# Optimization experiments

Measured on AMD Instinct MI355X. Metric: run time of the kernel, lower is better.

The kernel has to match this reference:

```python
import jax, jax.numpy as jnp
import numpy as np

B, D = 4096, 1024
NA, NNEG = 2048, 4094
L2_WEIGHT = 0.005


def setup_inputs() -> dict:
    key = jax.random.key(0)
    k1, k2, k3, k4 = jax.random.split(key, 4)
    batch = jax.random.normal(k1, (B, D), dtype=jnp.float32)
    anchors = jax.random.randint(k2, (NA,), 0, B)
    positives = jax.random.randint(k3, (NA,), 0, B)
    negatives = jax.random.randint(k4, (NA, NNEG), 0, B)
    return {"batch": batch, "anchors": anchors, "positives": positives, "negatives": negatives}


def reference(batch, anchors, positives, negatives):
    # a . (n - p) = a.n - a.p  -> one GEMM against the whole batch, then gathers.
    a_embs = batch[anchors]                       # [Na, D]
    scores = a_embs @ batch.T                     # [Na, B]
    pos = jnp.take_along_axis(scores, positives[:, None], axis=1)   # [Na, 1]
    neg = jnp.take_along_axis(scores, negatives, axis=1)            # [Na, Nneg]
    inner = neg - pos                             # [Na, Nneg]
    npair = jnp.mean(jnp.log(jnp.sum(jnp.exp(inner), axis=1) + 1.0))
    # per-anchor l2 term: l2_weight * mean(||batch||) added len(anchors) times / len(anchors)
    l2 = L2_WEIGHT * jnp.mean(jnp.linalg.norm(batch, axis=1))
    return npair + l2
```

## Files before the change

### kernel.cpp

```cpp
#include <hip/hip_runtime.h>
#include <hip/hip_bf16.h>
#include <math.h>

constexpr int kB    = 4096;
constexpr int kD    = 1024;
constexpr int kNA   = 2048;
constexpr int kNNEG = 4094;
constexpr float kL2W = 0.005f;


typedef __attribute__((ext_vector_type(8))) short short8;
typedef __attribute__((ext_vector_type(4))) float f32x4;

__device__ inline void async_load16(const void* g, void* l) {
    __builtin_amdgcn_global_load_lds(
        (const __attribute__((address_space(1))) unsigned*)g,
        (__attribute__((address_space(3))) unsigned*)l, 16, 0, 0);
}
__device__ inline float bf16_to_f(unsigned short u) {
    union { unsigned int i; float f; } c; c.i = ((unsigned int)u) << 16; return c.f;
}

__global__ __launch_bounds__(256) void conv_norms_kernel(
    const float* __restrict__ batch,
    unsigned short* __restrict__ bf,
    float* __restrict__ norms)
{
    const int row = blockIdx.x, t = threadIdx.x;
    const float4 v = ((const float4*)(batch + (size_t)row * kD))[t];
    ushort4 o;
    __hip_bfloat16 h0 = __float2bfloat16(v.x); o.x = *(unsigned short*)&h0;
    __hip_bfloat16 h1 = __float2bfloat16(v.y); o.y = *(unsigned short*)&h1;
    __hip_bfloat16 h2 = __float2bfloat16(v.z); o.z = *(unsigned short*)&h2;
    __hip_bfloat16 h3 = __float2bfloat16(v.w); o.w = *(unsigned short*)&h3;
    ((ushort4*)(bf + (size_t)row * kD))[t] = o;

    float acc = v.x * v.x + v.y * v.y + v.z * v.z + v.w * v.w;
    __shared__ float s[4];
    const int lane = t & 63, wid = t >> 6;
#pragma unroll
    for (int o2 = 32; o2; o2 >>= 1) acc += __shfl_down(acc, o2);
    if (lane == 0) s[wid] = acc;
    __syncthreads();
    if (t == 0) norms[row] = sqrtf(s[0] + s[1] + s[2] + s[3]);
}

__global__ __launch_bounds__(256) void gemm_mfma_kernel(
    const unsigned short* __restrict__ bf,
    const int*            __restrict__ anchors,
    unsigned short*       __restrict__ scores)
{
    __shared__ __align__(16) char As[128 * 64];
    __shared__ __align__(16) char Bs[128 * 64];

    const int t  = threadIdx.x;
    const int w  = t >> 6;
    const int l  = t & 63;
    const int m0 = blockIdx.y * 128;
    const int n0 = blockIdx.x * 128;

    const int r0 = w * 32 + (l >> 2);
    const int r1 = r0 + 16;
    const int p  = l & 3;
    const int g0 = (p ^ ((r0 >> 1) & 3)) * 8;
    const int g1 = (p ^ ((r1 >> 1) & 3)) * 8;

    const unsigned short* gA0 = bf + (size_t)anchors[m0 + r0] * kD + g0;
    const unsigned short* gA1 = bf + (size_t)anchors[m0 + r1] * kD + g1;
    const unsigned short* gB0 = bf + (size_t)(n0 + r0) * kD + g0;
    const unsigned short* gB1 = bf + (size_t)(n0 + r1) * kD + g1;

    char* lA0 = As + r0 * 64 + p * 16;
    char* lA1 = As + r1 * 64 + p * 16;
    char* lB0 = Bs + r0 * 64 + p * 16;
    char* lB1 = Bs + r1 * 64 + p * 16;

    const int wm = (w >> 1) * 64, wn = (w & 1) * 64;
    const int mr = l & 15, q = l >> 4;

    f32x4 acc[4][4] = {};

    for (int kt = 0; kt < kD; kt += 32) {
        async_load16(gA0 + kt, lA0);
        async_load16(gA1 + kt, lA1);
        async_load16(gB0 + kt, lB0);
        async_load16(gB1 + kt, lB1);
        __syncthreads();

        short8 a[4], b[4];
#pragma unroll
        for (int i = 0; i < 4; ++i) {
            const int mt = wm + i * 16 + mr;
            const int pc = q ^ ((mt >> 1) & 3);
            a[i] = *(const short8*)(As + mt * 64 + pc * 16);
            const int nt = wn + i * 16 + mr;
            const int pc2 = q ^ ((nt >> 1) & 3);
            b[i] = *(const short8*)(Bs + nt * 64 + pc2 * 16);
        }
#pragma unroll
        for (int i = 0; i < 4; ++i)
#pragma unroll
            for (int j = 0; j < 4; ++j)
                acc[i][j] = __builtin_amdgcn_mfma_f32_16x16x32_bf16(
                    a[i], b[j], acc[i][j], 0, 0, 0);
        __syncthreads();
    }

#pragma unroll
    for (int i = 0; i < 4; ++i)
#pragma unroll
        for (int j = 0; j < 4; ++j)
#pragma unroll
            for (int r = 0; r < 4; ++r) {
                const int row = m0 + wm + i * 16 + q * 4 + r;
                const int col = n0 + wn + j * 16 + mr;
                __hip_bfloat16 h = __float2bfloat16(acc[i][j][r]);
                scores[(size_t)row * kB + col] = *(unsigned short*)&h;
            }
}

__global__ __launch_bounds__(256) void lse_kernel(
    const unsigned short* __restrict__ scores,
    const int*   __restrict__ positives,
    const int*   __restrict__ negatives,
    float*       __restrict__ lse)
{
    __shared__ unsigned short srow[kB];
    const int i = blockIdx.x;
    const int t = threadIdx.x;

    const uint4* grow = (const uint4*)(scores + (size_t)i * kB);
    ((uint4*)srow)[t]       = grow[t];
    ((uint4*)srow)[t + 256] = grow[t + 256];
    __syncthreads();

    const float pos = bf16_to_f(srow[positives[i]]);
    const int* negrow = negatives + (size_t)i * kNNEG;

    float v[16];
    float m = -INFINITY;
#pragma unroll
    for (int r = 0; r < 16; ++r) {
        const int j = t + 256 * r;
        v[r] = (j < kNNEG) ? (bf16_to_f(srow[negrow[j]]) - pos) : -INFINITY;
        m = fmaxf(m, v[r]);
    }

    __shared__ float sm[4], ss[4];
    const int lane = t & 63, wid = t >> 6;
#pragma unroll
    for (int o = 32; o; o >>= 1) m = fmaxf(m, __shfl_down(m, o));
    if (lane == 0) sm[wid] = m;
    __syncthreads();
    m = fmaxf(fmaxf(sm[0], sm[1]), fmaxf(sm[2], sm[3]));
    const float mp = fmaxf(m, 0.f);

    float acc = 0.f;
#pragma unroll
    for (int r = 0; r < 16; ++r) acc += expf(v[r] - mp);

#pragma unroll
    for (int o = 32; o; o >>= 1) acc += __shfl_down(acc, o);
    if (lane == 0) ss[wid] = acc;
    __syncthreads();
    if (t == 0)
        lse[i] = mp + logf(ss[0] + ss[1] + ss[2] + ss[3] + expf(-mp));
}

__global__ __launch_bounds__(256) void final_kernel(
    const float* __restrict__ lse,
    const float* __restrict__ norms,
    float*       __restrict__ out)
{
    float a = 0.f, b = 0.f;
    for (int i = threadIdx.x; i < kNA; i += 256) a += lse[i];
    for (int i = threadIdx.x; i < kB;  i += 256) b += norms[i];
    __shared__ float sa[4], sb[4];
    const int lane = threadIdx.x & 63, wid = threadIdx.x >> 6;
#pragma unroll
    for (int o = 32; o; o >>= 1) { a += __shfl_down(a, o); b += __shfl_down(b, o); }
    if (lane == 0) { sa[wid] = a; sb[wid] = b; }
    __syncthreads();
    if (threadIdx.x == 0) {
        const float npair = (sa[0] + sa[1] + sa[2] + sa[3]) / (float)kNA;
        const float l2    = kL2W * ((sb[0] + sb[1] + sb[2] + sb[3]) / (float)kB);
        out[0] = npair + l2;
    }
}

extern "C" void kernel_launch(void* const* d_in, const int* in_sizes, int n_in,
                              void* d_out, int out_size, void* d_ws, size_t ws_size,
                              hipStream_t stream)
{
    (void)in_sizes; (void)n_in; (void)out_size; (void)ws_size;

    const float* batch     = (const float*)d_in[0];
    const int*   anchors   = (const int*)d_in[1];
    const int*   positives = (const int*)d_in[2];
    const int*   negatives = (const int*)d_in[3];
    float*       out       = (float*)d_out;

    char* ws = (char*)d_ws;
    unsigned short* scores = (unsigned short*)ws;
    unsigned short* bf     = (unsigned short*)(ws + (size_t)kNA * kB * 2);
    float*          lse    = (float*)(ws + (size_t)kNA * kB * 2 + (size_t)kB * kD * 2);
    float*          norms  = lse + kNA;

    conv_norms_kernel<<<kB, 256, 0, stream>>>(batch, bf, norms);
    gemm_mfma_kernel<<<dim3(kB / 128, kNA / 128), 256, 0, stream>>>(bf, anchors, scores);
    lse_kernel<<<kNA, 256, 0, stream>>>(scores, positives, negatives, lse);
    final_kernel<<<1, 256, 0, stream>>>(lse, norms, out);
}
```

Measured before the change: 125.9 us.

## Switch GEMM operands to FP8 and use scaled 16x16x128 MFMA

Converts the batch to FP8 (E4M3) instead of bf16 and runs the score GEMM with the MI355X scaled f8f6f4 MFMA at K=128 per step. The LDS tiles grow to 128 bytes per row with a new XOR swizzle, and anchor indices are cached in shared memory. This halves operand bytes and reduces the number of K iterations and syncs. It lowers precision of the scores, which may push error tolerance given the exp/log-sum over scores of magnitude ~D.

```diff
diff --git a/kernel.cpp b/kernel.cpp
--- a/kernel.cpp
+++ b/kernel.cpp
@@ -9,7 +9,8 @@
 constexpr float kL2W = 0.005f;
 
 
-typedef __attribute__((ext_vector_type(8))) short short8;
+typedef __attribute__((ext_vector_type(8))) int   int8v;
+typedef __attribute__((ext_vector_type(4))) int   int4v;
 typedef __attribute__((ext_vector_type(4))) float f32x4;
 
 __device__ inline void async_load16(const void* g, void* l) {
@@ -23,17 +24,14 @@
 
 __global__ __launch_bounds__(256) void conv_norms_kernel(
     const float* __restrict__ batch,
-    unsigned short* __restrict__ bf,
+    unsigned char* __restrict__ f8,
     float* __restrict__ norms)
 {
     const int row = blockIdx.x, t = threadIdx.x;
     const float4 v = ((const float4*)(batch + (size_t)row * kD))[t];
-    ushort4 o;
-    __hip_bfloat16 h0 = __float2bfloat16(v.x); o.x = *(unsigned short*)&h0;
-    __hip_bfloat16 h1 = __float2bfloat16(v.y); o.y = *(unsigned short*)&h1;
-    __hip_bfloat16 h2 = __float2bfloat16(v.z); o.z = *(unsigned short*)&h2;
-    __hip_bfloat16 h3 = __float2bfloat16(v.w); o.w = *(unsigned short*)&h3;
-    ((ushort4*)(bf + (size_t)row * kD))[t] = o;
+    unsigned int p = __builtin_amdgcn_cvt_pk_fp8_f32(v.x, v.y, 0, false);
+    p = __builtin_amdgcn_cvt_pk_fp8_f32(v.z, v.w, p, true);
+    ((unsigned int*)(f8 + (size_t)row * kD))[t] = p;
 
     float acc = v.x * v.x + v.y * v.y + v.z * v.z + v.w * v.w;
     __shared__ float s[4];
@@ -46,12 +44,13 @@
 }
 
 __global__ __launch_bounds__(256) void gemm_mfma_kernel(
-    const unsigned short* __restrict__ bf,
-    const int*            __restrict__ anchors,
-    unsigned short*       __restrict__ scores)
-{
-    __shared__ __align__(16) char As[128 * 64];
-    __shared__ __align__(16) char Bs[128 * 64];
+    const unsigned char* __restrict__ f8,
+    const int*           __restrict__ anchors,
+    unsigned short*      __restrict__ scores)
+{
+    __shared__ __align__(16) char As[128 * 128];
+    __shared__ __align__(16) char Bs[128 * 128];
+    __shared__ int aid[128];
 
     const int t  = threadIdx.x;
     const int w  = t >> 6;
@@ -59,50 +58,58 @@
     const int m0 = blockIdx.y * 128;
     const int n0 = blockIdx.x * 128;
 
-    const int r0 = w * 32 + (l >> 2);
-    const int r1 = r0 + 16;
-    const int p  = l & 3;
-    const int g0 = (p ^ ((r0 >> 1) & 3)) * 8;
-    const int g1 = (p ^ ((r1 >> 1) & 3)) * 8;
-
-    const unsigned short* gA0 = bf + (size_t)anchors[m0 + r0] * kD + g0;
-    const unsigned short* gA1 = bf + (size_t)anchors[m0 + r1] * kD + g1;
-    const unsigned short* gB0 = bf + (size_t)(n0 + r0) * kD + g0;
-    const unsigned short* gB1 = bf + (size_t)(n0 + r1) * kD + g1;
-
-    char* lA0 = As + r0 * 64 + p * 16;
-    char* lA1 = As + r1 * 64 + p * 16;
-    char* lB0 = Bs + r0 * 64 + p * 16;
-    char* lB1 = Bs + r1 * 64 + p * 16;
+    if (t < 128) aid[t] = anchors[m0 + t];
+    __syncthreads();
+
+    const unsigned char* gA[4];
+    const unsigned char* gB[4];
+    int slot[4];
+#pragma unroll
+    for (int i = 0; i < 4; ++i) {
+        const int idx = i * 256 + t;
+        const int row = idx >> 3;
+        const int pc  = idx & 7;
+        const int g   = pc ^ (row & 7);
+        gA[i]   = f8 + (size_t)aid[row] * kD + g * 16;
+        gB[i]   = f8 + (size_t)(n0 + row) * kD + g * 16;
+        slot[i] = idx * 16;
+    }
 
     const int wm = (w >> 1) * 64, wn = (w & 1) * 64;
     const int mr = l & 15, q = l >> 4;
 
     f32x4 acc[4][4] = {};
 
-    for (int kt = 0; kt < kD; kt += 32) {
-        async_load16(gA0 + kt, lA0);
-        async_load16(gA1 + kt, lA1);
-        async_load16(gB0 + kt, lB0);
-        async_load16(gB1 + kt, lB1);
+    for (int kt = 0; kt < kD; kt += 128) {
+#pragma unroll
+        for (int i = 0; i < 4; ++i) async_load16(gA[i] + kt, As + slot[i]);
+#pragma unroll
+        for (int i = 0; i < 4; ++i) async_load16(gB[i] + kt, Bs + slot[i]);
         __syncthreads();
 
-        short8 a[4], b[4];
+        int8v a[4], b[4];
 #pragma unroll
         for (int i = 0; i < 4; ++i) {
-            const int mt = wm + i * 16 + mr;
-            const int pc = q ^ ((mt >> 1) & 3);
-            a[i] = *(const short8*)(As + mt * 64 + pc * 16);
-            const int nt = wn + i * 16 + mr;
-            const int pc2 = q ^ ((nt >> 1) & 3);
-            b[i] = *(const short8*)(Bs + nt * 64 + pc2 * 16);
+            int r  = wm + i * 16 + mr;
+            int c0 = (2 * q) ^ (r & 7), c1 = (2 * q + 1) ^ (r & 7);
+            int4v lo = *(const int4v*)(As + r * 128 + c0 * 16);
+            int4v hi = *(const int4v*)(As + r * 128 + c1 * 16);
+            a[i] = (int8v){lo.x, lo.y, lo.z, lo.w, hi.x, hi.y, hi.z, hi.w};
+            r  = wn + i * 16 + mr;
+            c0 = (2 * q) ^ (r & 7); c1 = (2 * q + 1) ^ (r & 7);
+            lo = *(const int4v*)(Bs + r * 128 + c0 * 16);
+            hi = *(const int4v*)(Bs + r * 128 + c1 * 16);
+            b[i] = (int8v){lo.x, lo.y, lo.z, lo.w, hi.x, hi.y, hi.z, hi.w};
         }
 #pragma unroll
         for (int i = 0; i < 4; ++i)
 #pragma unroll
             for (int j = 0; j < 4; ++j)
-                acc[i][j] = __builtin_amdgcn_mfma_f32_16x16x32_bf16(
-                    a[i], b[j], acc[i][j], 0, 0, 0);
+                acc[i][j] = __builtin_amdgcn_mfma_scale_f32_16x16x128_f8f6f4(
+                    a[i], b[j], acc[i][j],
+                    0 , 0 ,
+                    0, 0x7F ,
+                    0, 0x7F );
         __syncthreads();
     }
 
@@ -202,12 +209,12 @@
 
     char* ws = (char*)d_ws;
     unsigned short* scores = (unsigned short*)ws;
-    unsigned short* bf     = (unsigned short*)(ws + (size_t)kNA * kB * 2);
-    float*          lse    = (float*)(ws + (size_t)kNA * kB * 2 + (size_t)kB * kD * 2);
+    unsigned char*  f8     = (unsigned char*)(ws + (size_t)kNA * kB * 2);
+    float*          lse    = (float*)(ws + (size_t)kNA * kB * 2 + (size_t)kB * kD);
     float*          norms  = lse + kNA;
 
-    conv_norms_kernel<<<kB, 256, 0, stream>>>(batch, bf, norms);
-    gemm_mfma_kernel<<<dim3(kB / 128, kNA / 128), 256, 0, stream>>>(bf, anchors, scores);
+    conv_norms_kernel<<<kB, 256, 0, stream>>>(batch, f8, norms);
+    gemm_mfma_kernel<<<dim3(kB / 128, kNA / 128), 256, 0, stream>>>(f8, anchors, scores);
     lse_kernel<<<kNA, 256, 0, stream>>>(scores, positives, negatives, lse);
     final_kernel<<<1, 256, 0, stream>>>(lse, norms, out);
 }
```

After: 116.6 us. 1.08x faster.
